# Kernel optimization log

Measured on AMD Instinct MI355X. Metric: run time of the kernel, lower is better.

Reference implementation:

```python
import jax, jax.numpy as jnp
import numpy as np

B, V, N, E, F = 32, 6, 128, 128, 128  # batch, visits(=6), neighbour_size, ninfeat, noutfeat
NREL = 11
ALPHA = 0.2  # LeakyReLU negative slope


def setup_inputs() -> dict:
    key = jax.random.key(0)
    k1, k2, k3, k4, k5, k6 = jax.random.split(key, 6)
    feature_embed = jax.random.normal(k1, (B, V, N, E), dtype=jnp.float32)
    neighbour_embed = jax.random.normal(k2, (B, V, N, E), dtype=jnp.float32)
    w_index = jax.random.randint(k3, (B, V, N), 0, NREL + 1)
    # 0/1 keep mask, as in the original (indicator is a 01 tensor)
    indicator = (jax.random.uniform(k4, (B, V, N)) > 0.2).astype(jnp.float32)
    # stacked relation weight matrices, xavier_uniform with gain 1.414
    limit = 1.414 * np.sqrt(6.0 / (E + F))
    W = jax.random.uniform(k5, (NREL + 1, E, F), minval=-limit, maxval=limit, dtype=jnp.float32)
    # nn.Linear(2F, 1, bias=False) weight, stored transposed: (2F, 1)
    lim_a = 1.0 / np.sqrt(2 * F)
    a = jax.random.uniform(k6, (2 * F, 1), minval=-lim_a, maxval=lim_a, dtype=jnp.float32)
    return {"feature_embed": feature_embed, "neighbour_embed": neighbour_embed,
            "w_index": w_index, "indicator": indicator, "W": W, "a": a}


def reference(feature_embed, neighbour_embed, w_index, indicator, W, a):
    # gather per-edge relation weight matrices: (B,V,N,E,F)  -- the memory-heavy step
    Wg = W[w_index]
    neighbour = jnp.einsum('bvne,bvnef->bvnf', neighbour_embed, Wg)
    feature = jnp.einsum('bvne,bvnef->bvnf', feature_embed, Wg)
    hh = jnp.concatenate([neighbour, feature], axis=-1)           # (B,V,N,2F)
    e = jax.nn.leaky_relu(hh @ a, negative_slope=ALPHA)           # (B,V,N,1)
    attn = jax.nn.softmax(e, axis=-2)                             # softmax over neighbours
    # dropout is identity in eval mode
    attn = attn * indicator[..., None]                            # mask
    return jnp.einsum('bvnj,bvnf->bvf', attn, neighbour)          # (B,V,F)
```

## Files before the change

kernel.cpp:

```cpp
#include <hip/hip_runtime.h>
#include <hip/hip_fp16.h>

#define NREL1  12
#define NN     128
#define EE     128
#define FF     128
#define BV     192
#define RK     (NREL1 * EE)

#define WS_WA  0
#define WS_WH  4096

__global__ __launch_bounds__(256) void prep_kernel(const float* __restrict__ W,
                                                   const float* __restrict__ a,
                                                   float* __restrict__ ws) {
    const int w    = blockIdx.x * 4 + (threadIdx.x >> 6);
    const int lane = threadIdx.x & 63;
    const int r = w >> 7, e = w & 127;
    const float2 wv = *(const float2*)(W + (size_t)(r * EE + e) * FF + lane * 2);
    const float2 a1 = *(const float2*)(a + lane * 2);
    const float2 a2 = *(const float2*)(a + FF + lane * 2);
    float d1 = wv.x * a1.x + wv.y * a1.y;
    float d2 = wv.x * a2.x + wv.y * a2.y;
#pragma unroll
    for (int off = 32; off; off >>= 1) {
        d1 += __shfl_xor(d1, off);
        d2 += __shfl_xor(d2, off);
    }
    if (lane == 0) {
        ws[WS_WA + r * EE + e]      = d1;
        ws[WS_WA + RK + r * EE + e] = d2;
    }
    const int gid = blockIdx.x * 256 + threadIdx.x;
    const float2 wv2 = *(const float2*)(W + (size_t)2 * gid);
    ((__half2*)(ws + WS_WH))[gid] = __float22half2_rn(wv2);
}

__global__ __launch_bounds__(1024) void gat_fused(const float* __restrict__ fe,
                                                  const float* __restrict__ ne,
                                                  const int* __restrict__ widx,
                                                  const float* __restrict__ ind,
                                                  const float* __restrict__ ws_r,
                                                  float* __restrict__ out) {
    __shared__ float wa[2 * RK];
    __shared__ float s16[16][RK];
    __shared__ float red[32][FF];
    __shared__ float red2[4][FF];
    __shared__ float e_lds[NN];

    const int bv   = blockIdx.x;
    const int tid  = threadIdx.x;
    const int wave = tid >> 6;
    const int lane = tid & 63;
    const int l32  = lane & 31;
    const int half = lane >> 5;

    const float* ne_bv = ne + (size_t)bv * NN * EE;
    const float* fe_bv = fe + (size_t)bv * NN * EE;

    float4 xn[4], xf[4];
    int    rr[4];
#pragma unroll
    for (int i = 0; i < 4; ++i) {
        const int n = wave * 8 + i * 2 + half;
        xn[i] = *(const float4*)(ne_bv + (size_t)n * EE + l32 * 4);
        xf[i] = *(const float4*)(fe_bv + (size_t)n * EE + l32 * 4);
        rr[i] = widx[bv * NN + n];
    }
    const float iv0 = ind[bv * NN + lane];
    const float iv1 = ind[bv * NN + lane + 64];

    if (tid < 2 * RK / 4)
        ((float4*)wa)[tid] = ((const float4*)(ws_r + WS_WA))[tid];
    {
        const float4 z = {0.f, 0.f, 0.f, 0.f};
#pragma unroll
        for (int q = 0; q < 6; ++q)
            ((float4*)&s16[0][0])[q * 1024 + tid] = z;
    }
    __syncthreads();

#pragma unroll
    for (int i = 0; i < 4; ++i) {
        const int n = wave * 8 + i * 2 + half;
        const float4 w1 = *(const float4*)&wa[rr[i] * EE + l32 * 4];
        const float4 w2 = *(const float4*)&wa[RK + rr[i] * EE + l32 * 4];
        float d = xn[i].x * w1.x + xn[i].y * w1.y + xn[i].z * w1.z + xn[i].w * w1.w
                + xf[i].x * w2.x + xf[i].y * w2.y + xf[i].z * w2.z + xf[i].w * w2.w;
#pragma unroll
        for (int off = 1; off <= 16; off <<= 1) d += __shfl_xor(d, off);
        if (l32 == 0) e_lds[n] = d > 0.f ? d : 0.2f * d;
    }
    __syncthreads();

    float a0, a1;
    {
        const float v0 = e_lds[lane], v1 = e_lds[lane + 64];
        float m = fmaxf(v0, v1);
#pragma unroll
        for (int off = 32; off; off >>= 1) m = fmaxf(m, __shfl_xor(m, off));
        const float ex0 = __expf(v0 - m), ex1 = __expf(v1 - m);
        float ss = ex0 + ex1;
#pragma unroll
        for (int off = 32; off; off >>= 1) ss += __shfl_xor(ss, off);
        const float inv = 1.f / ss;
        a0 = ex0 * inv * iv0;
        a1 = ex1 * inv * iv1;
    }

    float anv[4];
#pragma unroll
    for (int i = 0; i < 4; ++i) {
        const int n = wave * 8 + i * 2 + half;
        anv[i] = (wave < 8) ? __shfl(a0, n) : __shfl(a1, n - 64);
    }

    {
        float* sc = s16[wave];
        if (half == 0) {
#pragma unroll
            for (int i = 0; i < 4; ++i) {
                float* p = sc + rr[i] * EE + l32 * 4;
                float4 cur = *(const float4*)p;
                cur.x += anv[i] * xn[i].x; cur.y += anv[i] * xn[i].y;
                cur.z += anv[i] * xn[i].z; cur.w += anv[i] * xn[i].w;
                *(float4*)p = cur;
            }
        }
        __syncthreads();
        if (half == 1) {
#pragma unroll
            for (int i = 0; i < 4; ++i) {
                float* p = sc + rr[i] * EE + l32 * 4;
                float4 cur = *(const float4*)p;
                cur.x += anv[i] * xn[i].x; cur.y += anv[i] * xn[i].y;
                cur.z += anv[i] * xn[i].z; cur.w += anv[i] * xn[i].w;
                *(float4*)p = cur;
            }
        }
    }
    __syncthreads();

    if (tid < RK / 4) {
        float4 v = *(const float4*)&s16[0][tid * 4];
#pragma unroll
        for (int c = 1; c < 16; ++c) {
            const float4 t = *(const float4*)&s16[c][tid * 4];
            v.x += t.x; v.y += t.y; v.z += t.z; v.w += t.w;
        }
        *(float4*)&s16[0][tid * 4] = v;
    }
    __syncthreads();

    {
        const int fq = tid & 31;
        const int kg = tid >> 5;
        float4 sreg[12];
#pragma unroll
        for (int j = 0; j < 12; ++j)
            sreg[j] = *(const float4*)&s16[0][kg * 48 + j * 4];

        const __half* Wh = (const __half*)(ws_r + WS_WH);
        const __half* Wp = Wh + (size_t)(kg * 48) * FF + fq * 4;
        float4 acc = {0.f, 0.f, 0.f, 0.f};
#pragma unroll
        for (int j = 0; j < 12; ++j) {
#pragma unroll
            for (int u = 0; u < 4; ++u) {
                const float sv = (u == 0) ? sreg[j].x : (u == 1) ? sreg[j].y
                               : (u == 2) ? sreg[j].z : sreg[j].w;
                const float2 raw = *(const float2*)(Wp + (size_t)(j * 4 + u) * FF);
                const __half2* hp = (const __half2*)&raw;
                const float2 f01 = __half22float2(hp[0]);
                const float2 f23 = __half22float2(hp[1]);
                acc.x += sv * f01.x; acc.y += sv * f01.y;
                acc.z += sv * f23.x; acc.w += sv * f23.y;
            }
        }
        *(float4*)&red[kg][fq * 4] = acc;
    }
    __syncthreads();
    if (tid < 512) {
        const int f = tid & 127, h = tid >> 7;
        float v = 0.f;
#pragma unroll
        for (int j = 0; j < 8; ++j) v += red[h * 8 + j][f];
        red2[h][f] = v;
    }
    __syncthreads();
    if (tid < FF)
        out[bv * FF + tid] = red2[0][tid] + red2[1][tid] + red2[2][tid] + red2[3][tid];
}

extern "C" void kernel_launch(void* const* d_in, const int* in_sizes, int n_in,
                              void* d_out, int out_size, void* d_ws, size_t ws_size,
                              hipStream_t stream) {
    const float* fe  = (const float*)d_in[0];
    const float* ne  = (const float*)d_in[1];
    const int*   wi  = (const int*)d_in[2];
    const float* ind = (const float*)d_in[3];
    const float* W   = (const float*)d_in[4];
    const float* a   = (const float*)d_in[5];
    float* out = (float*)d_out;
    float* ws  = (float*)d_ws;

    prep_kernel<<<RK / 4, 256, 0, stream>>>(W, a, ws);
    gat_fused<<<BV, 1024, 0, stream>>>(fe, ne, wi, ind, ws, out);
}
```

Before: 23.68 us.

## Split attention and projection into separate kernels with batched fp16 W GEMM

The fused per-(b,v) kernel becomes three stages. Attention scatter now runs on two half-neighbour blocks per (b,v), doubling the block count. It computes unnormalized exp scores, accumulates the softmax denominator with a global atomicAdd, and writes per-relation partial sums to workspace. A new GEMM kernel processes 16 (b,v) rows at a time, so each fp16 W tile is read once per group instead of once per row, and it atomically adds denominator-scaled results into the output, which the prep kernel now zeroes. This trades an extra launch, workspace round-trips, output atomics and dropping the softmax max-subtraction (overflow risk for large scores) for better occupancy and far less repeated W traffic.

```diff
diff --git a/kernel.cpp b/kernel.cpp
--- a/kernel.cpp
+++ b/kernel.cpp
@@ -9,11 +9,14 @@
 #define RK     (NREL1 * EE)
 
 #define WS_WA  0
+#define WS_Z   3200
 #define WS_WH  4096
+#define WS_SP  102400
 
 __global__ __launch_bounds__(256) void prep_kernel(const float* __restrict__ W,
                                                    const float* __restrict__ a,
-                                                   float* __restrict__ ws) {
+                                                   float* __restrict__ ws,
+                                                   float* __restrict__ out) {
     const int w    = blockIdx.x * 4 + (threadIdx.x >> 6);
     const int lane = threadIdx.x & 63;
     const int r = w >> 7, e = w & 127;
@@ -34,26 +37,29 @@
     const int gid = blockIdx.x * 256 + threadIdx.x;
     const float2 wv2 = *(const float2*)(W + (size_t)2 * gid);
     ((__half2*)(ws + WS_WH))[gid] = __float22half2_rn(wv2);
-}
-
-__global__ __launch_bounds__(1024) void gat_fused(const float* __restrict__ fe,
-                                                  const float* __restrict__ ne,
-                                                  const int* __restrict__ widx,
-                                                  const float* __restrict__ ind,
-                                                  const float* __restrict__ ws_r,
-                                                  float* __restrict__ out) {
+    if (gid < BV * FF) out[gid] = 0.f;
+    if (gid < BV) ws[WS_Z + gid] = 0.f;
+}
+
+__global__ __launch_bounds__(512) void attn_part(const float* __restrict__ fe,
+                                                 const float* __restrict__ ne,
+                                                 const int* __restrict__ widx,
+                                                 const float* __restrict__ ind,
+                                                 float* __restrict__ ws) {
     __shared__ float wa[2 * RK];
-    __shared__ float s16[16][RK];
-    __shared__ float red[32][FF];
-    __shared__ float red2[4][FF];
-    __shared__ float e_lds[NN];
-
-    const int bv   = blockIdx.x;
+    __shared__ float s8[8][RK];
+    __shared__ float e_lds[64];
+    __shared__ float attn_lds[64];
+
+    const int blk  = blockIdx.x;
+    const int bv   = blk >> 1;
+    const int h    = blk & 1;
     const int tid  = threadIdx.x;
     const int wave = tid >> 6;
     const int lane = tid & 63;
     const int l32  = lane & 31;
     const int half = lane >> 5;
+    const int rot  = (blk * 38) & 62;
 
     const float* ne_bv = ne + (size_t)bv * NN * EE;
     const float* fe_bv = fe + (size_t)bv * NN * EE;
@@ -62,68 +68,57 @@
     int    rr[4];
 #pragma unroll
     for (int i = 0; i < 4; ++i) {
-        const int n = wave * 8 + i * 2 + half;
+        const int nl = (wave * 8 + i * 2 + half + rot) & 63;
+        const int n  = h * 64 + nl;
         xn[i] = *(const float4*)(ne_bv + (size_t)n * EE + l32 * 4);
         xf[i] = *(const float4*)(fe_bv + (size_t)n * EE + l32 * 4);
         rr[i] = widx[bv * NN + n];
     }
-    const float iv0 = ind[bv * NN + lane];
-    const float iv1 = ind[bv * NN + lane + 64];
-
-    if (tid < 2 * RK / 4)
-        ((float4*)wa)[tid] = ((const float4*)(ws_r + WS_WA))[tid];
+
+    for (int q = tid; q < 2 * RK / 4; q += 512)
+        ((float4*)wa)[q] = ((const float4*)(ws + WS_WA))[q];
     {
         const float4 z = {0.f, 0.f, 0.f, 0.f};
 #pragma unroll
         for (int q = 0; q < 6; ++q)
-            ((float4*)&s16[0][0])[q * 1024 + tid] = z;
+            ((float4*)&s8[0][0])[q * 512 + tid] = z;
     }
     __syncthreads();
 
 #pragma unroll
     for (int i = 0; i < 4; ++i) {
-        const int n = wave * 8 + i * 2 + half;
+        const int nl = (wave * 8 + i * 2 + half + rot) & 63;
         const float4 w1 = *(const float4*)&wa[rr[i] * EE + l32 * 4];
         const float4 w2 = *(const float4*)&wa[RK + rr[i] * EE + l32 * 4];
         float d = xn[i].x * w1.x + xn[i].y * w1.y + xn[i].z * w1.z + xn[i].w * w1.w
                 + xf[i].x * w2.x + xf[i].y * w2.y + xf[i].z * w2.z + xf[i].w * w2.w;
 #pragma unroll
         for (int off = 1; off <= 16; off <<= 1) d += __shfl_xor(d, off);
-        if (l32 == 0) e_lds[n] = d > 0.f ? d : 0.2f * d;
-    }
-    __syncthreads();
-
-    float a0, a1;
+        if (l32 == 0) e_lds[nl] = __expf(d > 0.f ? d : 0.2f * d);
+    }
+    __syncthreads();
+
+    if (wave == 0) {
+        float z = e_lds[lane];
+#pragma unroll
+        for (int off = 1; off <= 32; off <<= 1) z += __shfl_xor(z, off);
+        if (lane == 0) atomicAdd(&ws[WS_Z + bv], z);
+    } else if (wave == 1) {
+        attn_lds[lane] = e_lds[lane] * ind[bv * NN + h * 64 + lane];
+    }
+    __syncthreads();
+
     {
-        const float v0 = e_lds[lane], v1 = e_lds[lane + 64];
-        float m = fmaxf(v0, v1);
-#pragma unroll
-        for (int off = 32; off; off >>= 1) m = fmaxf(m, __shfl_xor(m, off));
-        const float ex0 = __expf(v0 - m), ex1 = __expf(v1 - m);
-        float ss = ex0 + ex1;
-#pragma unroll
-        for (int off = 32; off; off >>= 1) ss += __shfl_xor(ss, off);
-        const float inv = 1.f / ss;
-        a0 = ex0 * inv * iv0;
-        a1 = ex1 * inv * iv1;
-    }
-
-    float anv[4];
-#pragma unroll
-    for (int i = 0; i < 4; ++i) {
-        const int n = wave * 8 + i * 2 + half;
-        anv[i] = (wave < 8) ? __shfl(a0, n) : __shfl(a1, n - 64);
-    }
-
-    {
-        float* sc = s16[wave];
+        float* sc = s8[wave];
         if (half == 0) {
 #pragma unroll
             for (int i = 0; i < 4; ++i) {
+                const int nl = (wave * 8 + i * 2 + rot) & 63;
+                const float an = attn_lds[nl];
                 float* p = sc + rr[i] * EE + l32 * 4;
                 float4 cur = *(const float4*)p;
-                cur.x += anv[i] * xn[i].x; cur.y += anv[i] * xn[i].y;
-                cur.z += anv[i] * xn[i].z; cur.w += anv[i] * xn[i].w;
+                cur.x += an * xn[i].x; cur.y += an * xn[i].y;
+                cur.z += an * xn[i].z; cur.w += an * xn[i].w;
                 *(float4*)p = cur;
             }
         }
@@ -131,10 +126,12 @@
         if (half == 1) {
 #pragma unroll
             for (int i = 0; i < 4; ++i) {
+                const int nl = (wave * 8 + i * 2 + 1 + rot) & 63;
+                const float an = attn_lds[nl];
                 float* p = sc + rr[i] * EE + l32 * 4;
                 float4 cur = *(const float4*)p;
-                cur.x += anv[i] * xn[i].x; cur.y += anv[i] * xn[i].y;
-                cur.z += anv[i] * xn[i].z; cur.w += anv[i] * xn[i].w;
+                cur.x += an * xn[i].x; cur.y += an * xn[i].y;
+                cur.z += an * xn[i].z; cur.w += an * xn[i].w;
                 *(float4*)p = cur;
             }
         }
@@ -142,54 +139,73 @@
     __syncthreads();
 
     if (tid < RK / 4) {
-        float4 v = *(const float4*)&s16[0][tid * 4];
-#pragma unroll
-        for (int c = 1; c < 16; ++c) {
-            const float4 t = *(const float4*)&s16[c][tid * 4];
+        float4 v = *(const float4*)&s8[0][tid * 4];
+#pragma unroll
+        for (int c = 1; c < 8; ++c) {
+            const float4 t = *(const float4*)&s8[c][tid * 4];
             v.x += t.x; v.y += t.y; v.z += t.z; v.w += t.w;
         }
-        *(float4*)&s16[0][tid * 4] = v;
-    }
-    __syncthreads();
-
-    {
-        const int fq = tid & 31;
-        const int kg = tid >> 5;
-        float4 sreg[12];
-#pragma unroll
-        for (int j = 0; j < 12; ++j)
-            sreg[j] = *(const float4*)&s16[0][kg * 48 + j * 4];
-
-        const __half* Wh = (const __half*)(ws_r + WS_WH);
-        const __half* Wp = Wh + (size_t)(kg * 48) * FF + fq * 4;
-        float4 acc = {0.f, 0.f, 0.f, 0.f};
-#pragma unroll
-        for (int j = 0; j < 12; ++j) {
-#pragma unroll
-            for (int u = 0; u < 4; ++u) {
-                const float sv = (u == 0) ? sreg[j].x : (u == 1) ? sreg[j].y
-                               : (u == 2) ? sreg[j].z : sreg[j].w;
-                const float2 raw = *(const float2*)(Wp + (size_t)(j * 4 + u) * FF);
-                const __half2* hp = (const __half2*)&raw;
-                const float2 f01 = __half22float2(hp[0]);
-                const float2 f23 = __half22float2(hp[1]);
-                acc.x += sv * f01.x; acc.y += sv * f01.y;
-                acc.z += sv * f23.x; acc.w += sv * f23.y;
-            }
-        }
-        *(float4*)&red[kg][fq * 4] = acc;
-    }
-    __syncthreads();
-    if (tid < 512) {
-        const int f = tid & 127, h = tid >> 7;
-        float v = 0.f;
-#pragma unroll
-        for (int j = 0; j < 8; ++j) v += red[h * 8 + j][f];
-        red2[h][f] = v;
-    }
-    __syncthreads();
-    if (tid < FF)
-        out[bv * FF + tid] = red2[0][tid] + red2[1][tid] + red2[2][tid] + red2[3][tid];
+        *(float4*)(ws + WS_SP + (size_t)blk * RK + tid * 4) = v;
+    }
+}
+
+__global__ __launch_bounds__(256) void gemm_scale(const float* __restrict__ ws,
+                                                  float* __restrict__ out) {
+    __shared__ float st[128][20];
+    __shared__ float zinv[16];
+
+    const int bv0 = blockIdx.x * 16;
+    const int k0  = blockIdx.y * 128;
+    const int tid = threadIdx.x;
+
+    if (tid < 16) zinv[tid] = 1.f / ws[WS_Z + bv0 + tid];
+
+#pragma unroll
+    for (int qq = tid; qq < 512; qq += 256) {
+        const int b = qq >> 5, kk4 = qq & 31;
+        const float* base = ws + WS_SP + (size_t)(bv0 + b) * 2 * RK + k0 + kk4 * 4;
+        const float4 v0 = *(const float4*)(base);
+        const float4 v1 = *(const float4*)(base + RK);
+        st[kk4 * 4 + 0][b] = v0.x + v1.x;
+        st[kk4 * 4 + 1][b] = v0.y + v1.y;
+        st[kk4 * 4 + 2][b] = v0.z + v1.z;
+        st[kk4 * 4 + 3][b] = v0.w + v1.w;
+    }
+    __syncthreads();
+
+    const int fq = tid & 31;
+    const int bg = (tid >> 5) & 3;
+    const int kh = tid >> 7;
+
+    float4 acc[4] = {{0,0,0,0},{0,0,0,0},{0,0,0,0},{0,0,0,0}};
+    const __half* Wh = (const __half*)(ws + WS_WH);
+    const __half* Wp = Wh + (size_t)(k0 + kh * 64) * FF + fq * 4;
+
+#pragma unroll 4
+    for (int k = 0; k < 64; ++k) {
+        const float2 raw = *(const float2*)(Wp + (size_t)k * FF);
+        const __half2* hp = (const __half2*)&raw;
+        const float2 f01 = __half22float2(hp[0]);
+        const float2 f23 = __half22float2(hp[1]);
+        const float* sp = &st[kh * 64 + k][bg * 4];
+#pragma unroll
+        for (int j = 0; j < 4; ++j) {
+            const float sv = sp[j];
+            acc[j].x += sv * f01.x; acc[j].y += sv * f01.y;
+            acc[j].z += sv * f23.x; acc[j].w += sv * f23.y;
+        }
+    }
+
+#pragma unroll
+    for (int j = 0; j < 4; ++j) {
+        const int b = bg * 4 + j;
+        const float zi = zinv[b];
+        float* op = out + (size_t)(bv0 + b) * FF + fq * 4;
+        atomicAdd(op + 0, acc[j].x * zi);
+        atomicAdd(op + 1, acc[j].y * zi);
+        atomicAdd(op + 2, acc[j].z * zi);
+        atomicAdd(op + 3, acc[j].w * zi);
+    }
 }
 
 extern "C" void kernel_launch(void* const* d_in, const int* in_sizes, int n_in,
@@ -204,6 +220,7 @@
     float* out = (float*)d_out;
     float* ws  = (float*)d_ws;
 
-    prep_kernel<<<RK / 4, 256, 0, stream>>>(W, a, ws);
-    gat_fused<<<BV, 1024, 0, stream>>>(fe, ne, wi, ind, ws, out);
-}
+    prep_kernel<<<RK / 4, 256, 0, stream>>>(W, a, ws, out);
+    attn_part<<<BV * 2, 512, 0, stream>>>(fe, ne, wi, ind, ws);
+    gemm_scale<<<dim3(12, 12), 256, 0, stream>>>(ws, out);
+}
```

Result: slower. 32.30 us (+36.4%).
